# Optimization experiments

Measured on AMD Instinct MI355X. Metric: run time of the kernel, lower is better.

The kernel has to match this reference:

```python
import jax, jax.numpy as jnp
import numpy as np

DIM = 16      # must equal K*K per the module's reshape structure
K = 4         # kernel_size
HEADS = 8
SCALE = (DIM // HEADS) ** (-0.5)


def setup_inputs() -> dict:
    key = jax.random.key(0)
    k1, k2 = jax.random.split(key)
    x = jax.random.normal(k1, (2, 64, 67, 67), dtype=jnp.float32)
    # torch Linear(dim, 3*dim, bias=False) weight: [3*dim, dim]
    w_qkv = jax.random.normal(k2, (3 * DIM, DIM), dtype=jnp.float32) * 0.1
    return {"x": x, "w_qkv": w_qkv}


def reference(x, w_qkv):
    B, C, H, W = x.shape
    k = K
    Ho, Wo = H - k + 1, W - k + 1          # unfold output grid (stride=1)
    L = Ho * Wo
    # Unfold: patches[b, c, i*k+j, ph, pw] = x[b, c, ph+i, pw+j]
    # (matches torch F.unfold channel ordering c-major, then i, then j)
    patches = jnp.stack(
        [x[:, :, i:i + Ho, j:j + Wo] for i in range(k) for j in range(k)],
        axis=2,
    )  # [B, C, k*k, Ho, Wo]
    seq = L // (k * k)                      # L must be divisible by k*k
    # [B*C*k*k, seq, k*k] -- flatten (Ho,Wo)->L row-major then split into (seq, k*k)
    xu = patches.reshape(B * C * k * k, seq, k * k)
    # tiny attention over each row; feature dim = k*k = DIM
    qkv = xu @ w_qkv.T                      # [N, seq, 3*DIM]
    q, kk_, v = jnp.split(qkv, 3, axis=-1)
    scores = jnp.einsum('nqd,nkd->nqk', q, kk_) * SCALE   # [N, seq, seq]
    attn = jax.nn.softmax(scores, axis=-1)                # dropout = identity (eval)
    ao = jnp.einsum('nqk,nkd->nqd', attn, v)              # [N, seq, DIM]
    ao = ao.reshape(B, C, k, k, Ho, Wo)
    # overlap-add fold back onto the HxW grid
    out = jnp.zeros_like(x)
    for i in range(k):
        for j in range(k):
            out = out.at[:, :, i:Ho + i, j:Wo + j].add(ao[:, :, i, j])
    return out
```

## Files before the change

kernel.cpp:

```cpp
#include <hip/hip_runtime.h>


#define BATCH 2
#define CHAN 64
#define HWDIM 67
#define SEQ 256
#define DIM 16
#define NSEQ 2048
#define PLANE 4096
#define OUT_TOTAL (BATCH * CHAN * HWDIM * HWDIM)
#define ATT_SCALE 0.70710678118654752f
#define LOG2E 1.44269504088896340736f

typedef _Float16 half4 __attribute__((ext_vector_type(4)));
typedef _Float16 half8 __attribute__((ext_vector_type(8)));
typedef float float4v __attribute__((ext_vector_type(4)));

static __device__ __forceinline__ half4 pack4(float4v c) {
    half4 h;
    h[0] = (_Float16)c[0]; h[1] = (_Float16)c[1];
    h[2] = (_Float16)c[2]; h[3] = (_Float16)c[3];
    return h;
}

__global__ __launch_bounds__(256, 4) void ska_attn_pass1(
    const float* __restrict__ x,
    const float* __restrict__ w,
    _Float16* __restrict__ ao)
{
    __shared__ _Float16 xF[16][64][4];
    __shared__ _Float16 kvA[16][64][8];

    const int n  = blockIdx.x;
    const int p  = n & 15;
    const int bc = n >> 4;
    const int oi = p >> 2;
    const int oj = p & 3;

    const int s   = threadIdx.x;
    const int ph  = s >> 2;
    const int pw0 = (s & 3) * DIM;

    const float* xrow = x + ((size_t)bc * HWDIM + (ph + oi)) * HWDIM + pw0 + oj;
    const int kt = s >> 4, kk = s & 15;
#pragma unroll
    for (int dh = 0; dh < 4; ++dh) {
        half4 h;
#pragma unroll
        for (int r = 0; r < 4; ++r) h[r] = (_Float16)xrow[4 * dh + r];
        *(half4*)&xF[kt][kk + 16 * dh][0] = h;
    }

    const int wave = s >> 6;
    const int lane = s & 63;
    const int o = lane & 15;
    const int g = lane >> 4;

    const float4 wq4 = *(const float4*)(w + ( 0 + o) * DIM + 4 * g);
    const float4 wk4 = *(const float4*)(w + (16 + o) * DIM + 4 * g);
    const float4 wv4 = *(const float4*)(w + (32 + o) * DIM + 4 * g);
    half4 wqf, wkf, wvf;
    wqf[0] = (_Float16)(wq4.x * (ATT_SCALE * LOG2E));
    wqf[1] = (_Float16)(wq4.y * (ATT_SCALE * LOG2E));
    wqf[2] = (_Float16)(wq4.z * (ATT_SCALE * LOG2E));
    wqf[3] = (_Float16)(wq4.w * (ATT_SCALE * LOG2E));
    wkf[0] = (_Float16)wk4.x; wkf[1] = (_Float16)wk4.y;
    wkf[2] = (_Float16)wk4.z; wkf[3] = (_Float16)wk4.w;
    wvf[0] = (_Float16)wv4.x; wvf[1] = (_Float16)wv4.y;
    wvf[2] = (_Float16)wv4.z; wvf[3] = (_Float16)wv4.w;

    const float4v zf = (float4v){0.f, 0.f, 0.f, 0.f};

    half4 qfr[4];
#pragma unroll
    for (int u = 0; u < 4; ++u) {
        const int t = 4 * wave + u;
        const half4 xf = *(const half4*)&xF[t][lane][0];
        const half4 kf = pack4(__builtin_amdgcn_mfma_f32_16x16x16f16(wkf, xf, zf, 0, 0, 0));
        const half4 vf = pack4(__builtin_amdgcn_mfma_f32_16x16x16f16(xf, wvf, zf, 0, 0, 0));
        half8 kv;
        kv[0] = kf[0]; kv[1] = kf[1]; kv[2] = kf[2]; kv[3] = kf[3];
        kv[4] = vf[0]; kv[5] = vf[1]; kv[6] = vf[2]; kv[7] = vf[3];
        *(half8*)&kvA[t][lane][0] = kv;
        qfr[u] = pack4(__builtin_amdgcn_mfma_f32_16x16x16f16(wqf, xf, zf, 0, 0, 0));
    }
    __syncthreads();

    float4v oacc[4];
    float lpart[4];
#pragma unroll
    for (int j = 0; j < 4; ++j) {
        oacc[j] = zf;
        lpart[j] = 0.f;
    }

#pragma unroll 4
    for (int t = 0; t < 16; ++t) {
        const half8 kv = *(const half8*)&kvA[t][lane][0];
        half4 kf, vf;
        kf[0] = kv[0]; kf[1] = kv[1]; kf[2] = kv[2]; kf[3] = kv[3];
        vf[0] = kv[4]; vf[1] = kv[5]; vf[2] = kv[6]; vf[3] = kv[7];
#pragma unroll
        for (int j = 0; j < 4; ++j) {
            float4v sfr = __builtin_amdgcn_mfma_f32_16x16x16f16(kf, qfr[j], zf, 0, 0, 0);
            const float p0 = __builtin_amdgcn_exp2f(sfr[0]);
            const float p1 = __builtin_amdgcn_exp2f(sfr[1]);
            const float p2 = __builtin_amdgcn_exp2f(sfr[2]);
            const float p3 = __builtin_amdgcn_exp2f(sfr[3]);
            lpart[j] += (p0 + p1) + (p2 + p3);
            half4 pb;
            pb[0] = (_Float16)p0; pb[1] = (_Float16)p1;
            pb[2] = (_Float16)p2; pb[3] = (_Float16)p3;
            oacc[j] = __builtin_amdgcn_mfma_f32_16x16x16f16(vf, pb, oacc[j], 0, 0, 0);
        }
    }

#pragma unroll
    for (int j = 0; j < 4; ++j) {
        float lj = lpart[j];
        lj += __shfl_xor(lj, 16, 64);
        lj += __shfl_xor(lj, 32, 64);
        const float rl = 1.f / lj;
        const int query = (4 * wave + j) * 16 + (lane & 15);
        half4 hv;
        hv[0] = (_Float16)(oacc[j][0] * rl);
        hv[1] = (_Float16)(oacc[j][1] * rl);
        hv[2] = (_Float16)(oacc[j][2] * rl);
        hv[3] = (_Float16)(oacc[j][3] * rl);
        *(half4*)(ao + (size_t)n * PLANE + query * DIM + 4 * g) = hv;
    }
}

__global__ __launch_bounds__(256) void ska_fold_pass2(
    const _Float16* __restrict__ ao,
    float* __restrict__ out)
{
    const int idx = blockIdx.x * 256 + threadIdx.x;
    if (idx >= OUT_TOTAL) return;
    const int w  = idx % HWDIM;
    const int t  = idx / HWDIM;
    const int h  = t % HWDIM;
    const int bc = t / HWDIM;

    const _Float16* base = ao + (size_t)bc * 16 * PLANE;
    float acc = 0.f;
#pragma unroll
    for (int i = 0; i < 4; ++i) {
        const int ph = h - i;
        if (ph < 0 || ph >= 64) continue;
#pragma unroll
        for (int j = 0; j < 4; ++j) {
            const int pw = w - j;
            if (pw < 0 || pw >= 64) continue;
            acc += (float)base[(i * 4 + j) * PLANE + ph * 64 + pw];
        }
    }
    out[idx] = acc;
}

__global__ __launch_bounds__(256) void ska_attn_atomic(
    const float* __restrict__ x, const float* __restrict__ w,
    float* __restrict__ out)
{
    __shared__ float sw[3 * DIM * DIM];
    __shared__ float sk[SEQ][DIM];
    __shared__ float sv[SEQ][DIM];

    const int n = blockIdx.x, p = n & 15, bc = n >> 4, oi = p >> 2, oj = p & 3;
    const int s = threadIdx.x, ph = s >> 2, pw0 = (s & 3) * DIM;

#pragma unroll
    for (int r = 0; r < 3; ++r) sw[r * 256 + s] = w[r * 256 + s];

    const float* xrow = x + ((size_t)bc * HWDIM + (ph + oi)) * HWDIM + pw0 + oj;
    float xr[DIM];
#pragma unroll
    for (int d = 0; d < DIM; ++d) xr[d] = xrow[d];
    __syncthreads();

    float q[DIM];
#pragma unroll
    for (int o = 0; o < DIM; ++o) {
        float aq = 0.f, ak = 0.f, av = 0.f;
#pragma unroll
        for (int d = 0; d < DIM; ++d) {
            aq += xr[d] * sw[o * DIM + d];
            ak += xr[d] * sw[(DIM + o) * DIM + d];
            av += xr[d] * sw[(2 * DIM + o) * DIM + d];
        }
        q[o] = aq * ATT_SCALE; sk[s][o] = ak; sv[s][o] = av;
    }
    __syncthreads();

    float l = 0.f, acc[DIM];
#pragma unroll
    for (int d = 0; d < DIM; ++d) acc[d] = 0.f;
    for (int t = 0; t < SEQ; ++t) {
        float sc = 0.f;
#pragma unroll
        for (int d = 0; d < DIM; ++d) sc += q[d] * sk[t][d];
        const float pe = __expf(sc);
        l += pe;
#pragma unroll
        for (int d = 0; d < DIM; ++d) acc[d] += pe * sv[t][d];
    }
    const float rl = 1.f / l;
    float* obase = out + ((size_t)bc * HWDIM + (ph + oi)) * HWDIM + pw0 + oj;
#pragma unroll
    for (int d = 0; d < DIM; ++d) atomicAdd(&obase[d], acc[d] * rl);
}

extern "C" void kernel_launch(void* const* d_in, const int* in_sizes, int n_in,
                              void* d_out, int out_size, void* d_ws, size_t ws_size,
                              hipStream_t stream) {
    const float* x = (const float*)d_in[0];
    const float* w = (const float*)d_in[1];
    float* out = (float*)d_out;

    const size_t need = (size_t)NSEQ * PLANE * sizeof(_Float16);
    if (ws_size >= need) {
        _Float16* ao = (_Float16*)d_ws;
        ska_attn_pass1<<<NSEQ, 256, 0, stream>>>(x, w, ao);
        ska_fold_pass2<<<(OUT_TOTAL + 255) / 256, 256, 0, stream>>>(ao, out);
    } else {
        (void)hipMemsetAsync(out, 0, (size_t)out_size * sizeof(float), stream);
        ska_attn_atomic<<<NSEQ, 256, 0, stream>>>(x, w, out);
    }
}
```

Baseline: 92.77 us.

## Stage fold rows in LDS and alias pass1 shared buffers for occupancy

The fold kernel now gives each block one (b,c) plane and four output rows. It loads the needed rows of all 16 patch planes into shared memory with vectorized half8 loads, then sums the 16 contributions per pixel from LDS. Before, each output pixel gathered 16 scattered global half loads with per-pixel div/mod. Pass1 also reuses one shared buffer for the x tile and the K/V tile and raises its occupancy hint from 4 to 8 blocks per CU, trading LDS footprint for more resident waves.

```diff
diff --git a/kernel.cpp b/kernel.cpp
--- a/kernel.cpp
+++ b/kernel.cpp
@@ -11,6 +11,7 @@
 #define OUT_TOTAL (BATCH * CHAN * HWDIM * HWDIM)
 #define ATT_SCALE 0.70710678118654752f
 #define LOG2E 1.44269504088896340736f
+#define HTILES 17
 
 typedef _Float16 half4 __attribute__((ext_vector_type(4)));
 typedef _Float16 half8 __attribute__((ext_vector_type(8)));
@@ -23,13 +24,12 @@
     return h;
 }
 
-__global__ __launch_bounds__(256, 4) void ska_attn_pass1(
+__global__ __launch_bounds__(256, 8) void ska_attn_pass1(
     const float* __restrict__ x,
     const float* __restrict__ w,
     _Float16* __restrict__ ao)
 {
-    __shared__ _Float16 xF[16][64][4];
-    __shared__ _Float16 kvA[16][64][8];
+    __shared__ _Float16 buf[16][64][8];
 
     const int n  = blockIdx.x;
     const int p  = n & 15;
@@ -48,7 +48,7 @@
         half4 h;
 #pragma unroll
         for (int r = 0; r < 4; ++r) h[r] = (_Float16)xrow[4 * dh + r];
-        *(half4*)&xF[kt][kk + 16 * dh][0] = h;
+        *(half4*)&buf[kt][kk + 16 * dh][0] = h;
     }
 
     const int wave = s >> 6;
@@ -75,13 +75,13 @@
 #pragma unroll
     for (int u = 0; u < 4; ++u) {
         const int t = 4 * wave + u;
-        const half4 xf = *(const half4*)&xF[t][lane][0];
+        const half4 xf = *(const half4*)&buf[t][lane][0];
         const half4 kf = pack4(__builtin_amdgcn_mfma_f32_16x16x16f16(wkf, xf, zf, 0, 0, 0));
         const half4 vf = pack4(__builtin_amdgcn_mfma_f32_16x16x16f16(xf, wvf, zf, 0, 0, 0));
         half8 kv;
         kv[0] = kf[0]; kv[1] = kf[1]; kv[2] = kf[2]; kv[3] = kf[3];
         kv[4] = vf[0]; kv[5] = vf[1]; kv[6] = vf[2]; kv[7] = vf[3];
-        *(half8*)&kvA[t][lane][0] = kv;
+        *(half8*)&buf[t][lane][0] = kv;
         qfr[u] = pack4(__builtin_amdgcn_mfma_f32_16x16x16f16(wqf, xf, zf, 0, 0, 0));
     }
     __syncthreads();
@@ -96,7 +96,7 @@
 
 #pragma unroll 4
     for (int t = 0; t < 16; ++t) {
-        const half8 kv = *(const half8*)&kvA[t][lane][0];
+        const half8 kv = *(const half8*)&buf[t][lane][0];
         half4 kf, vf;
         kf[0] = kv[0]; kf[1] = kv[1]; kf[2] = kv[2]; kf[3] = kv[3];
         vf[0] = kv[4]; vf[1] = kv[5]; vf[2] = kv[6]; vf[3] = kv[7];
@@ -135,27 +135,50 @@
     const _Float16* __restrict__ ao,
     float* __restrict__ out)
 {
-    const int idx = blockIdx.x * 256 + threadIdx.x;
-    if (idx >= OUT_TOTAL) return;
-    const int w  = idx % HWDIM;
-    const int t  = idx / HWDIM;
-    const int h  = t % HWDIM;
-    const int bc = t / HWDIM;
-
-    const _Float16* base = ao + (size_t)bc * 16 * PLANE;
-    float acc = 0.f;
-#pragma unroll
-    for (int i = 0; i < 4; ++i) {
-        const int ph = h - i;
-        if (ph < 0 || ph >= 64) continue;
-#pragma unroll
-        for (int j = 0; j < 4; ++j) {
-            const int pw = w - j;
-            if (pw < 0 || pw >= 64) continue;
-            acc += (float)base[(i * 4 + j) * PLANE + ph * 64 + pw];
-        }
-    }
-    out[idx] = acc;
+    __shared__ _Float16 sA[16][4][64];
+
+    const int blk = blockIdx.x;
+    const int h0  = (blk % HTILES) * 4;
+    const int bc  = blk / HTILES;
+    const int tid = threadIdx.x;
+
+    {
+        const int pl = tid >> 4;
+        const int hh = (tid >> 2) & 3;
+        const int pw = (tid & 3) * 16;
+        const int i  = pl >> 2;
+        const int prow = h0 + hh - i;
+        half8 v0, v1;
+        if (prow >= 0 && prow < 64) {
+            const _Float16* src = ao + ((size_t)(bc * 16 + pl)) * PLANE + prow * 64 + pw;
+            v0 = *(const half8*)src;
+            v1 = *(const half8*)(src + 8);
+        } else {
+            const half8 z = (half8)(_Float16)0.f;
+            v0 = z; v1 = z;
+        }
+        *(half8*)&sA[pl][hh][pw]     = v0;
+        *(half8*)&sA[pl][hh][pw + 8] = v1;
+    }
+    __syncthreads();
+
+    for (int px = tid; px < 4 * HWDIM; px += 256) {
+        const int hh = px / HWDIM;
+        const int ww = px % HWDIM;
+        const int h  = h0 + hh;
+        if (h >= HWDIM) continue;
+        float acc = 0.f;
+#pragma unroll
+        for (int i = 0; i < 4; ++i) {
+#pragma unroll
+            for (int j = 0; j < 4; ++j) {
+                const int pw = ww - j;
+                if (pw < 0 || pw >= 64) continue;
+                acc += (float)sA[i * 4 + j][hh][pw];
+            }
+        }
+        out[((size_t)bc * HWDIM + h) * HWDIM + ww] = acc;
+    }
 }
 
 __global__ __launch_bounds__(256) void ska_attn_atomic(
@@ -221,7 +244,7 @@
     if (ws_size >= need) {
         _Float16* ao = (_Float16*)d_ws;
         ska_attn_pass1<<<NSEQ, 256, 0, stream>>>(x, w, ao);
-        ska_fold_pass2<<<(OUT_TOTAL + 255) / 256, 256, 0, stream>>>(ao, out);
+        ska_fold_pass2<<<BATCH * CHAN * HTILES, 256, 0, stream>>>(ao, out);
     } else {
         (void)hipMemsetAsync(out, 0, (size_t)out_size * sizeof(float), stream);
         ska_attn_atomic<<<NSEQ, 256, 0, stream>>>(x, w, out);
```

Result: faster. 88.86 us (-4.2%).
